# Optimization experiments

Measured on AMD Instinct MI355X. Metric: run time of the kernel, lower is better.

The kernel has to match this reference:

```python
import jax, jax.numpy as jnp
import numpy as np

B, N = 2, 384
NODE_DIM, NODE_HIDDEN, EDGE_DIM = 128, 256, 64
EDGE_H1 = 2 * EDGE_DIM + 2 * NODE_DIM  # 384, forced by concat in edge update
EDGE_H2 = 128
HEADS = 8
SCALE = 1.0 / float(np.sqrt(NODE_HIDDEN // HEADS))  # torch uses node_hidden//heads
EPS = 1e-5


def _w(k, out_dim, in_dim):
    return jax.random.normal(k, (out_dim, in_dim), dtype=jnp.float32) * 0.02


def setup_inputs() -> dict:
    ks = jax.random.split(jax.random.key(0), 32)
    inp = {
        'x': jax.random.normal(ks[0], (B, N, NODE_DIM), dtype=jnp.float32),
        'dense_adj': jax.random.normal(ks[1], (B, N, N, EDGE_DIM), dtype=jnp.float32),
        'wnq': _w(ks[2], NODE_DIM, NODE_DIM),
        'wnk': _w(ks[3], NODE_DIM, NODE_DIM),
        'wnv': _w(ks[4], NODE_DIM, NODE_DIM),
        'weq': _w(ks[5], NODE_DIM, EDGE_DIM),
        'wek': _w(ks[6], NODE_DIM, EDGE_DIM),
        'wev': _w(ks[7], NODE_DIM, EDGE_DIM),
        'nfc1_w': _w(ks[8], NODE_DIM, NODE_DIM),
        'nfc1_b': jnp.zeros((NODE_DIM,), jnp.float32),
        'ln1_g': jnp.ones((NODE_DIM,), jnp.float32),
        'ln1_b': jnp.zeros((NODE_DIM,), jnp.float32),
        'nfc2_w': _w(ks[9], NODE_HIDDEN, NODE_DIM),
        'nfc2_b': jnp.zeros((NODE_HIDDEN,), jnp.float32),
        'nfc3_w': _w(ks[10], NODE_DIM, NODE_HIDDEN),
        'nfc3_b': jnp.zeros((NODE_DIM,), jnp.float32),
        'ln2_g': jnp.ones((NODE_DIM,), jnp.float32),
        'ln2_b': jnp.zeros((NODE_DIM,), jnp.float32),
        'efc1_w': _w(ks[11], EDGE_DIM, EDGE_H1),
        'efc1_b': jnp.zeros((EDGE_DIM,), jnp.float32),
        'efc2_w': _w(ks[12], EDGE_DIM, EDGE_DIM),
        'efc2_b': jnp.zeros((EDGE_DIM,), jnp.float32),
        'eln1_g': jnp.ones((EDGE_DIM,), jnp.float32),
        'eln1_b': jnp.zeros((EDGE_DIM,), jnp.float32),
        'efc3_w': _w(ks[13], EDGE_H2, EDGE_DIM),
        'efc3_b': jnp.zeros((EDGE_H2,), jnp.float32),
        'efc4_w': _w(ks[14], EDGE_DIM, EDGE_H2),
        'efc4_b': jnp.zeros((EDGE_DIM,), jnp.float32),
        'eln2_g': jnp.ones((EDGE_DIM,), jnp.float32),
        'eln2_b': jnp.zeros((EDGE_DIM,), jnp.float32),
    }
    return inp


def layer_norm(t, g, b):
    m = jnp.mean(t, axis=-1, keepdims=True)
    v = jnp.mean((t - m) ** 2, axis=-1, keepdims=True)
    return (t - m) * jax.lax.rsqrt(v + EPS) * g + b


def rt_attention(x, adj, wnq, wnk, wnv, weq, wek, wev):
    Bb, Nn, D = x.shape
    d = D // HEADS
    def sn(t):  # [B,N,D] -> [B,H,N,d]
        return t.reshape(Bb, Nn, HEADS, d).transpose(0, 2, 1, 3)
    def se(t):  # [B,N,N,D] -> [B,H,N,N,d]
        return t.reshape(Bb, Nn, Nn, HEADS, d).transpose(0, 3, 1, 2, 4)
    # edge-augmented per-pair q,k,v: [B,H,i,j,d]
    q = sn(x @ wnq.T)[:, :, :, None, :] + se(adj @ weq.T)
    k = sn(x @ wnk.T)[:, :, None, :, :] + se(adj @ wek.T)
    v = sn(x @ wnv.T)[:, :, None, :, :] + se(adj @ wev.T)
    scores = jnp.sum(q * k, axis=-1) * SCALE          # [B,H,i,j]
    attn = jax.nn.softmax(scores, axis=-1)            # softmax over keys j
    out = jnp.einsum('bhij,bhijc->bhic', attn, v)     # [B,H,N,d]
    # torch reshape_from_batches interleaves as [B,N,d,H] -> [B,N,d*H]
    return out.transpose(0, 2, 3, 1).reshape(Bb, Nn, D)


def reference(x, dense_adj, wnq, wnk, wnv, weq, wek, wev,
              nfc1_w, nfc1_b, ln1_g, ln1_b, nfc2_w, nfc2_b, nfc3_w, nfc3_b,
              ln2_g, ln2_b, efc1_w, efc1_b, efc2_w, efc2_b, eln1_g, eln1_b,
              efc3_w, efc3_b, efc4_w, efc4_b, eln2_g, eln2_b):
    attn_out = rt_attention(x, dense_adj, wnq, wnk, wnv, weq, wek, wev)
    res = attn_out @ nfc1_w.T + nfc1_b
    x = layer_norm(x + res, ln1_g, ln1_b)
    res = jax.nn.relu(x @ nfc2_w.T + nfc2_b) @ nfc3_w.T + nfc3_b
    x = layer_norm(x + res, ln2_g, ln2_b)
    # edge update: [adj_ij, adj_ji, x_j (source), x_i (target)]
    Bb, Nn, D = x.shape
    src = jnp.broadcast_to(x[:, None, :, :], (Bb, Nn, Nn, D))
    tgt = jnp.broadcast_to(x[:, :, None, :], (Bb, Nn, Nn, D))
    rev = jnp.swapaxes(dense_adj, -2, -3)
    ua = jnp.concatenate([dense_adj, rev, src, tgt], axis=-1)  # [B,N,N,EDGE_H1]
    res = jax.nn.relu(ua @ efc1_w.T + efc1_b) @ efc2_w.T + efc2_b
    adj = layer_norm(dense_adj + res, eln1_g, eln1_b)
    res = jax.nn.relu(adj @ efc3_w.T + efc3_b) @ efc4_w.T + efc4_b
    adj = layer_norm(adj + res, eln2_g, eln2_b)
    return (x, adj)
```

## Files before the change

kernel.cpp:

```cpp
#include <hip/hip_runtime.h>
#include <hip/hip_bf16.h>

typedef unsigned short u16;
typedef unsigned int u32;

#define NB 2
#define NN 384
#define ND 128
#define NE 64
#define NHD 8
#define NHID 256
#define EH1 384
#define EH2 128
#define LN_EPS 1e-5f
#define ATT_SCALE 0.17677669529663687f

#define XOUT_ELEMS (NB * NN * ND)
#define ADJ_ELEMS ((size_t)NB * NN * NN * NE)
#define OUT_ELEMS (XOUT_ELEMS + ADJ_ELEMS)
#define SCRATCH_F32 (4 * XOUT_ELEMS)

typedef __attribute__((ext_vector_type(4))) float f32x4;
typedef __attribute__((ext_vector_type(8))) short s16x8;
#define MFMA16(a, b, c) __builtin_amdgcn_mfma_f32_16x16x32_bf16(a, b, c, 0, 0, 0)

__device__ __forceinline__ float bflo(u32 u) {
  return __builtin_bit_cast(float, u << 16);
}
__device__ __forceinline__ float bfhi(u32 u) {
  return __builtin_bit_cast(float, u & 0xffff0000u);
}
__device__ __forceinline__ u16 bfr(float f) {
  return __builtin_bit_cast(u16, __float2bfloat16(f));
}
__device__ __forceinline__ float bfu(u16 h) {
  return __builtin_bit_cast(float, ((u32)h) << 16);
}
__device__ __forceinline__ u32 packbf(float a, float b) {
  return (u32)bfr(a) | ((u32)bfr(b) << 16);
}
__device__ __forceinline__ float wsum64(float v) {
#pragma unroll
  for (int o = 32; o > 0; o >>= 1) v += __shfl_xor(v, o, 64);
  return v;
}
__device__ __forceinline__ float wmax64(float v) {
#pragma unroll
  for (int o = 32; o > 0; o >>= 1) v = fmaxf(v, __shfl_xor(v, o, 64));
  return v;
}

__device__ __forceinline__ s16x8 cvt_frag(const float* p) {
  float4 a = *(const float4*)p;
  float4 c = *(const float4*)(p + 4);
  s16x8 r;
  r[0] = (short)bfr(a.x); r[1] = (short)bfr(a.y);
  r[2] = (short)bfr(a.z); r[3] = (short)bfr(a.w);
  r[4] = (short)bfr(c.x); r[5] = (short)bfr(c.y);
  r[6] = (short)bfr(c.z); r[7] = (short)bfr(c.w);
  return r;
}

__device__ __forceinline__ void cvt8_hl(const float* p, uint4& hi, uint4& lo) {
  float4 a = *(const float4*)p;
  float4 c = *(const float4*)(p + 4);
  float v[8] = {a.x, a.y, a.z, a.w, c.x, c.y, c.z, c.w};
  u32 hw[4], lw[4];
#pragma unroll
  for (int e = 0; e < 4; ++e) {
    u16 h0 = bfr(v[2 * e]), h1 = bfr(v[2 * e + 1]);
    u16 l0 = bfr(v[2 * e] - bfu(h0));
    u16 l1 = bfr(v[2 * e + 1] - bfu(h1));
    hw[e] = (u32)h0 | ((u32)h1 << 16);
    lw[e] = (u32)l0 | ((u32)l1 << 16);
  }
  hi.x = hw[0]; hi.y = hw[1]; hi.z = hw[2]; hi.w = hw[3];
  lo.x = lw[0]; lo.y = lw[1]; lo.z = lw[2]; lo.w = lw[3];
}

__global__ void k_node_qkv(const float* __restrict__ x,
                           const float* __restrict__ wq,
                           const float* __restrict__ wk,
                           const float* __restrict__ wv,
                           float* __restrict__ nq, float* __restrict__ nk,
                           float* __restrict__ nv) {
  int row = blockIdx.x;
  int t = threadIdx.x;
  __shared__ float xs[ND];
  xs[t] = x[row * ND + t];
  __syncthreads();
  float aq = 0.f, ak = 0.f, av = 0.f;
  for (int k = 0; k < ND; ++k) {
    float xv = xs[k];
    aq += xv * wq[t * ND + k];
    ak += xv * wk[t * ND + k];
    av += xv * wv[t * ND + k];
  }
  nq[row * ND + t] = aq;
  nk[row * ND + t] = ak;
  nv[row * ND + t] = av;
}

#define ATJ 128
struct AttnS {
  u16 Ahi[ATJ][NE];
  u16 Alo[ATJ][NE];
  float sc[NHD][NN];
  float psum[NHD][NE];
  float part[4][ND];
};

__global__ void __launch_bounds__(512) k_attn(
    const float* __restrict__ adj,
    const float* __restrict__ weq,
    const float* __restrict__ wek,
    const float* __restrict__ wev,
    const float* __restrict__ nq,
    const float* __restrict__ nk,
    const float* __restrict__ nv,
    float* __restrict__ att) {
  __shared__ AttnS s;
  int bi = blockIdx.x;
  int b = bi / NN;
  int t = threadIdx.x;
  int h = t >> 6;
  int l = t & 63;
  int lr = l & 15, lk = l >> 4;

  s16x8 BQ[2], BK[2];
  {
    const float* wqp = weq + (size_t)(h * 16 + lr) * NE + lk * 8;
    const float* wkp = wek + (size_t)(h * 16 + lr) * NE + lk * 8;
    BQ[0] = cvt_frag(wqp); BQ[1] = cvt_frag(wqp + 32);
    BK[0] = cvt_frag(wkp); BK[1] = cvt_frag(wkp + 32);
  }
  float nqd = nq[(size_t)bi * ND + h * 16 + lr];

  for (int tile = 0; tile < NN / ATJ; ++tile) {
    int jbase = tile * ATJ;
    __syncthreads();
    for (int p = t; p < ATJ * 8; p += 512) {
      int row = p >> 3, u = p & 7;
      const float* src = adj + ((size_t)bi * NN + jbase + row) * NE + u * 8;
      uint4 hi, lo;
      cvt8_hl(src, hi, lo);
      int byt = (row * 128 + u * 16) ^ ((row & 7) << 4);
      *(uint4*)((char*)s.Ahi + byt) = hi;
      *(uint4*)((char*)s.Alo + byt) = lo;
    }
    __syncthreads();

#pragma unroll
    for (int sub = 0; sub < ATJ / 16; ++sub) {
      int trow = sub * 16 + lr;
      int swz = (trow & 7) << 4;
      f32x4 eq = {0.f, 0.f, 0.f, 0.f}, ek = {0.f, 0.f, 0.f, 0.f};
#pragma unroll
      for (int ks = 0; ks < 2; ++ks) {
        int byt = (trow * 128 + ks * 64 + lk * 16) ^ swz;
        s16x8 ah = *(const s16x8*)((const char*)s.Ahi + byt);
        s16x8 al = *(const s16x8*)((const char*)s.Alo + byt);
        eq = MFMA16(ah, BQ[ks], eq);
        eq = MFMA16(al, BQ[ks], eq);
        ek = MFMA16(ah, BK[ks], ek);
        ek = MFMA16(al, BK[ks], ek);
      }
#pragma unroll
      for (int r = 0; r < 4; ++r) {
        int j = jbase + sub * 16 + lk * 4 + r;
        float kv = nk[((size_t)b * NN + j) * ND + h * 16 + lr] + ek[r];
        float prod = (nqd + eq[r]) * kv;
#pragma unroll
        for (int o = 8; o > 0; o >>= 1) prod += __shfl_xor(prod, o, 64);
        if (lr == 0) s.sc[h][j] = prod * ATT_SCALE;
      }
    }
  }
  __syncthreads();

  {
    float vals[NN / 64];
    float m = -1e30f;
#pragma unroll
    for (int r = 0; r < NN / 64; ++r) {
      vals[r] = s.sc[h][l + 64 * r];
      m = fmaxf(m, vals[r]);
    }
    m = wmax64(m);
    float sum = 0.f;
#pragma unroll
    for (int r = 0; r < NN / 64; ++r) {
      vals[r] = __expf(vals[r] - m);
      sum += vals[r];
    }
    sum = wsum64(sum);
    float rinv = 1.f / sum;
#pragma unroll
    for (int r = 0; r < NN / 64; ++r) s.sc[h][l + 64 * r] = vals[r] * rinv;
  }

  {
    float pacc = 0.f;
    const float* ab = adj + (size_t)bi * NN * NE + l;
    const float* prow = s.sc[h];
#pragma unroll 4
    for (int j = 0; j < NN; ++j) pacc += prow[j] * ab[(size_t)j * NE];
    s.psum[h][l] = pacc;
  }
  __syncthreads();

  {
    int c = t & 127, grp = t >> 7;
    int hc = c >> 4;
    float acc = 0.f;
    const float* nvb = nv + (size_t)b * NN * ND + c;
    const float* pr = s.sc[hc];
#pragma unroll 4
    for (int j = grp * (NN / 4); j < (grp + 1) * (NN / 4); ++j)
      acc += pr[j] * nvb[(size_t)j * ND];
    s.part[grp][c] = acc;
  }
  __syncthreads();
  if (t < ND) {
    int c = t, hc = c >> 4;
    float acc = s.part[0][c] + s.part[1][c] + s.part[2][c] + s.part[3][c];
    const float4* wr = (const float4*)(wev + c * NE);
    const float* ps = s.psum[hc];
#pragma unroll
    for (int k4 = 0; k4 < NE / 4; ++k4) {
      float4 w4 = wr[k4];
      acc += w4.x * ps[4 * k4] + w4.y * ps[4 * k4 + 1] +
             w4.z * ps[4 * k4 + 2] + w4.w * ps[4 * k4 + 3];
    }
    att[(size_t)bi * ND + (c & 15) * NHD + hc] = acc;
  }
}

struct FfnS {
  float atts[ND];
  float tvb[ND];
  float x1[ND];
  float hb[NHID];
  float stats[2];
};

__global__ void k_node_ffn(const float* __restrict__ x,
                           const float* __restrict__ att,
                           const float* __restrict__ w1, const float* __restrict__ b1,
                           const float* __restrict__ g1, const float* __restrict__ bb1,
                           const float* __restrict__ w2, const float* __restrict__ b2,
                           const float* __restrict__ w3, const float* __restrict__ b3,
                           const float* __restrict__ g2, const float* __restrict__ bb2,
                           float* __restrict__ xout) {
  __shared__ FfnS s;
  int row = blockIdx.x;
  int tid = threadIdx.x;
  if (tid < ND) s.atts[tid] = att[row * ND + tid];
  __syncthreads();

  if (tid < ND) {
    float acc = b1[tid];
    for (int k = 0; k < ND; ++k) acc += s.atts[k] * w1[tid * ND + k];
    s.tvb[tid] = x[row * ND + tid] + acc;
  }
  __syncthreads();
  if (tid == 0) {
    float m = 0.f;
    for (int k = 0; k < ND; ++k) m += s.tvb[k];
    m *= (1.f / ND);
    float v = 0.f;
    for (int k = 0; k < ND; ++k) { float d = s.tvb[k] - m; v += d * d; }
    s.stats[0] = m;
    s.stats[1] = rsqrtf(v * (1.f / ND) + LN_EPS);
  }
  __syncthreads();
  if (tid < ND)
    s.x1[tid] = (s.tvb[tid] - s.stats[0]) * s.stats[1] * g1[tid] + bb1[tid];
  __syncthreads();

  {
    float acc = b2[tid];
    for (int k = 0; k < ND; ++k) acc += s.x1[k] * w2[tid * ND + k];
    s.hb[tid] = fmaxf(acc, 0.f);
  }
  __syncthreads();

  if (tid < ND) {
    float acc = b3[tid];
    for (int k = 0; k < NHID; ++k) acc += s.hb[k] * w3[tid * NHID + k];
    s.tvb[tid] = s.x1[tid] + acc;
  }
  __syncthreads();
  if (tid == 0) {
    float m = 0.f;
    for (int k = 0; k < ND; ++k) m += s.tvb[k];
    m *= (1.f / ND);
    float v = 0.f;
    for (int k = 0; k < ND; ++k) { float d = s.tvb[k] - m; v += d * d; }
    s.stats[0] = m;
    s.stats[1] = rsqrtf(v * (1.f / ND) + LN_EPS);
  }
  __syncthreads();
  if (tid < ND) {
    float o = (s.tvb[tid] - s.stats[0]) * s.stats[1] * g2[tid] + bb2[tid];
    xout[row * ND + tid] = o;
  }
}

#define EMT 32

struct E1M {
  u16 Ahi[EMT][EH1];
  u16 Alo[EMT][EH1];
  u16 Hhi[EMT][NE];
  u16 Hlo[EMT][NE];
};

__global__ void __launch_bounds__(512) k_edge1(
    const float* __restrict__ adj, const float* __restrict__ xq,
    const float* __restrict__ w1, const float* __restrict__ b1,
    const float* __restrict__ w2, const float* __restrict__ b2,
    const float* __restrict__ g, const float* __restrict__ bb,
    float* __restrict__ adj1out) {
  __shared__ E1M s;
  int bi = blockIdx.x;
  int b = bi / NN, i = bi % NN;
  int t = threadIdx.x;
  int w = t >> 6, l = t & 63;
  int m16 = (w & 1) * 16;
  int n16 = (w >> 1) * 16;
  int lr = l & 15, lk = l >> 4;

  s16x8 B1[12], B2[2];
  {
    const float* wr = w1 + (size_t)(n16 + lr) * EH1 + lk * 8;
#pragma unroll
    for (int ks = 0; ks < 12; ++ks) B1[ks] = cvt_frag(wr + ks * 32);
    const float* w2r = w2 + (size_t)(n16 + lr) * NE + lk * 8;
#pragma unroll
    for (int ks = 0; ks < 2; ++ks) B2[ks] = cvt_frag(w2r + ks * 32);
  }
  float bias1 = b1[n16 + lr];
  float bias2 = b2[n16 + lr];
  float gl = g[l], bl = bb[l];

  for (int mt = 0; mt < NN / EMT; ++mt) {
    int jbase = mt * EMT;
    __syncthreads();
    for (int p = t; p < EMT * 48; p += 512) {
      int row = p / 48, u = p % 48;
      const float* src;
      if (u < 8)
        src = adj + ((size_t)bi * NN + jbase + row) * NE + u * 8;
      else if (u < 16)
        src = adj + ((size_t)(b * NN + jbase + row) * NN + i) * NE + (u - 8) * 8;
      else if (u < 32)
        src = xq + (size_t)(b * NN + jbase + row) * ND + (u - 16) * 8;
      else
        src = xq + (size_t)bi * ND + (u - 32) * 8;
      uint4 hi, lo;
      cvt8_hl(src, hi, lo);
      int byt = (row * 768 + u * 16) ^ ((row & 7) << 4);
      *(uint4*)((char*)s.Ahi + byt) = hi;
      *(uint4*)((char*)s.Alo + byt) = lo;
    }
    __syncthreads();

    f32x4 acc = {0.f, 0.f, 0.f, 0.f};
    int arow = m16 + lr;
    int aswz = (arow & 7) << 4;
#pragma unroll
    for (int ks = 0; ks < 12; ++ks) {
      int byt = (arow * 768 + ks * 64 + lk * 16) ^ aswz;
      s16x8 ah = *(const s16x8*)((const char*)s.Ahi + byt);
      s16x8 al = *(const s16x8*)((const char*)s.Alo + byt);
      acc = MFMA16(ah, B1[ks], acc);
      acc = MFMA16(al, B1[ks], acc);
    }
#pragma unroll
    for (int r = 0; r < 4; ++r) {
      float hv = fmaxf(acc[r] + bias1, 0.f);
      u16 hh = bfr(hv);
      u16 hl = bfr(hv - bfu(hh));
      int row = m16 + lk * 4 + r;
      int byt = (row * 128 + (n16 + lr) * 2) ^ ((row & 7) << 4);
      *(u16*)((char*)s.Hhi + byt) = hh;
      *(u16*)((char*)s.Hlo + byt) = hl;
    }
    __syncthreads();

    f32x4 acc2 = {0.f, 0.f, 0.f, 0.f};
#pragma unroll
    for (int ks = 0; ks < 2; ++ks) {
      int byt = (arow * 128 + ks * 64 + lk * 16) ^ aswz;
      s16x8 ah = *(const s16x8*)((const char*)s.Hhi + byt);
      s16x8 al = *(const s16x8*)((const char*)s.Hlo + byt);
      acc2 = MFMA16(ah, B2[ks], acc2);
      acc2 = MFMA16(al, B2[ks], acc2);
    }
    __syncthreads();
    float* tvb = (float*)s.Hhi;
#pragma unroll
    for (int r = 0; r < 4; ++r) {
      int row = m16 + lk * 4 + r;
      int col = n16 + lr;
      int abyt = (row * 768 + col * 2) ^ ((row & 7) << 4);
      float aorig = bfu(*(const u16*)((const char*)s.Ahi + abyt)) +
                    bfu(*(const u16*)((const char*)s.Alo + abyt));
      tvb[row * NE + col] = aorig + acc2[r] + bias2;
    }
    __syncthreads();
#pragma unroll
    for (int rr = 0; rr < EMT / 8; ++rr) {
      int row = w * (EMT / 8) + rr;
      float tv = tvb[row * NE + l];
      float mean = wsum64(tv) * (1.f / NE);
      float dv = tv - mean;
      float var = wsum64(dv * dv) * (1.f / NE);
      float o = dv * rsqrtf(var + LN_EPS) * gl + bl;
      adj1out[((size_t)bi * NN + jbase + row) * NE + l] = o;
    }
  }
}

struct E2M {
  u16 Ahi[EMT][NE];
  u16 Alo[EMT][NE];
  u16 Hhi[EMT][EH2];
  u16 Hlo[EMT][EH2];
};

__global__ void __launch_bounds__(512) k_edge2(
    float* __restrict__ adjio,
    const float* __restrict__ w3, const float* __restrict__ b3,
    const float* __restrict__ w4, const float* __restrict__ b4,
    const float* __restrict__ g, const float* __restrict__ bb) {
  __shared__ E2M s;
  int bi = blockIdx.x;
  int t = threadIdx.x;
  int w = t >> 6, l = t & 63;
  int m16 = (w & 1) * 16;
  int nb = (w >> 1) * 2;
  int n16 = (w >> 1) * 16;
  int lr = l & 15, lk = l >> 4;

  s16x8 B3[2][2], B4[4];
  {
#pragma unroll
    for (int n = 0; n < 2; ++n) {
      const float* wr = w3 + (size_t)((nb + n) * 16 + lr) * NE + lk * 8;
#pragma unroll
      for (int ks = 0; ks < 2; ++ks) B3[n][ks] = cvt_frag(wr + ks * 32);
    }
    const float* w4r = w4 + (size_t)(n16 + lr) * EH2 + lk * 8;
#pragma unroll
    for (int ks = 0; ks < 4; ++ks) B4[ks] = cvt_frag(w4r + ks * 32);
  }
  float bias3[2] = {b3[nb * 16 + lr], b3[(nb + 1) * 16 + lr]};
  float bias4 = b4[n16 + lr];
  float gl = g[l], bl = bb[l];

  for (int mt = 0; mt < NN / EMT; ++mt) {
    int jbase = mt * EMT;
    __syncthreads();
    for (int p = t; p < EMT * 8; p += 512) {
      int row = p >> 3, u = p & 7;
      const float* src = adjio + ((size_t)bi * NN + jbase + row) * NE + u * 8;
      uint4 hi, lo;
      cvt8_hl(src, hi, lo);
      int byt = (row * 128 + u * 16) ^ ((row & 7) << 4);
      *(uint4*)((char*)s.Ahi + byt) = hi;
      *(uint4*)((char*)s.Alo + byt) = lo;
    }
    __syncthreads();

    f32x4 a3[2] = {{0.f, 0.f, 0.f, 0.f}, {0.f, 0.f, 0.f, 0.f}};
    int arow = m16 + lr;
    int aswz = (arow & 7) << 4;
#pragma unroll
    for (int ks = 0; ks < 2; ++ks) {
      int byt = (arow * 128 + ks * 64 + lk * 16) ^ aswz;
      s16x8 ah = *(const s16x8*)((const char*)s.Ahi + byt);
      s16x8 al = *(const s16x8*)((const char*)s.Alo + byt);
#pragma unroll
      for (int n = 0; n < 2; ++n) {
        a3[n] = MFMA16(ah, B3[n][ks], a3[n]);
        a3[n] = MFMA16(al, B3[n][ks], a3[n]);
      }
    }
#pragma unroll
    for (int n = 0; n < 2; ++n) {
#pragma unroll
      for (int r = 0; r < 4; ++r) {
        float hv = fmaxf(a3[n][r] + bias3[n], 0.f);
        u16 hh = bfr(hv);
        u16 hl = bfr(hv - bfu(hh));
        int row = m16 + lk * 4 + r;
        int byt = (row * 256 + ((nb + n) * 16 + lr) * 2) ^ ((row & 7) << 4);
        *(u16*)((char*)s.Hhi + byt) = hh;
        *(u16*)((char*)s.Hlo + byt) = hl;
      }
    }
    __syncthreads();

    f32x4 a4 = {0.f, 0.f, 0.f, 0.f};
#pragma unroll
    for (int ks = 0; ks < 4; ++ks) {
      int byt = (arow * 256 + ks * 64 + lk * 16) ^ aswz;
      s16x8 ah = *(const s16x8*)((const char*)s.Hhi + byt);
      s16x8 al = *(const s16x8*)((const char*)s.Hlo + byt);
      a4 = MFMA16(ah, B4[ks], a4);
      a4 = MFMA16(al, B4[ks], a4);
    }
    __syncthreads();
    float* tvb = (float*)s.Hhi;
#pragma unroll
    for (int r = 0; r < 4; ++r) {
      int row = m16 + lk * 4 + r;
      int col = n16 + lr;
      int abyt = (row * 128 + col * 2) ^ ((row & 7) << 4);
      float aorig = bfu(*(const u16*)((const char*)s.Ahi + abyt)) +
                    bfu(*(const u16*)((const char*)s.Alo + abyt));
      tvb[row * NE + col] = aorig + a4[r] + bias4;
    }
    __syncthreads();
#pragma unroll
    for (int rr = 0; rr < EMT / 8; ++rr) {
      int row = w * (EMT / 8) + rr;
      float tv = tvb[row * NE + l];
      float mean = wsum64(tv) * (1.f / NE);
      float dv = tv - mean;
      float var = wsum64(dv * dv) * (1.f / NE);
      float o = dv * rsqrtf(var + LN_EPS) * gl + bl;
      adjio[((size_t)bi * NN + jbase + row) * NE + l] = o;
    }
  }
}

extern "C" void kernel_launch(void* const* d_in, const int* in_sizes, int n_in,
                              void* d_out, int out_size, void* d_ws, size_t ws_size,
                              hipStream_t stream) {
  (void)in_sizes; (void)n_in; (void)out_size; (void)d_ws; (void)ws_size;
  const float* x      = (const float*)d_in[0];
  const float* adj    = (const float*)d_in[1];
  const float* wnq    = (const float*)d_in[2];
  const float* wnk    = (const float*)d_in[3];
  const float* wnv    = (const float*)d_in[4];
  const float* weq    = (const float*)d_in[5];
  const float* wek    = (const float*)d_in[6];
  const float* wev    = (const float*)d_in[7];
  const float* nfc1_w = (const float*)d_in[8];
  const float* nfc1_b = (const float*)d_in[9];
  const float* ln1_g  = (const float*)d_in[10];
  const float* ln1_b  = (const float*)d_in[11];
  const float* nfc2_w = (const float*)d_in[12];
  const float* nfc2_b = (const float*)d_in[13];
  const float* nfc3_w = (const float*)d_in[14];
  const float* nfc3_b = (const float*)d_in[15];
  const float* ln2_g  = (const float*)d_in[16];
  const float* ln2_b  = (const float*)d_in[17];
  const float* efc1_w = (const float*)d_in[18];
  const float* efc1_b = (const float*)d_in[19];
  const float* efc2_w = (const float*)d_in[20];
  const float* efc2_b = (const float*)d_in[21];
  const float* eln1_g = (const float*)d_in[22];
  const float* eln1_b = (const float*)d_in[23];
  const float* efc3_w = (const float*)d_in[24];
  const float* efc3_b = (const float*)d_in[25];
  const float* efc4_w = (const float*)d_in[26];
  const float* efc4_b = (const float*)d_in[27];
  const float* eln2_g = (const float*)d_in[28];
  const float* eln2_b = (const float*)d_in[29];

  float* outf = (float*)d_out;
  float* outadj = outf + XOUT_ELEMS;

  float* scratch = outf + OUT_ELEMS - SCRATCH_F32;
  float* nq  = scratch;
  float* nk  = scratch + XOUT_ELEMS;
  float* nv  = scratch + 2 * XOUT_ELEMS;
  float* att = scratch + 3 * XOUT_ELEMS;

  k_node_qkv<<<NB * NN, 128, 0, stream>>>(x, wnq, wnk, wnv, nq, nk, nv);
  k_attn<<<NB * NN, 512, 0, stream>>>(adj, weq, wek, wev, nq, nk, nv, att);
  k_node_ffn<<<NB * NN, 256, 0, stream>>>(x, att, nfc1_w, nfc1_b, ln1_g, ln1_b,
                                          nfc2_w, nfc2_b, nfc3_w, nfc3_b,
                                          ln2_g, ln2_b, outf);
  k_edge1<<<NB * NN, 512, 0, stream>>>(adj, outf, efc1_w, efc1_b, efc2_w, efc2_b,
                                       eln1_g, eln1_b, outadj);
  k_edge2<<<NB * NN, 512, 0, stream>>>(outadj, efc3_w, efc3_b, efc4_w, efc4_b,
                                       eln2_g, eln2_b);
}
```

Baseline: 620.4 us.

## Fuse edge MLP stages into one kernel and fold target-node term into bias

Merges the two edge kernels into a single kernel, so the intermediate layer-normed adjacency stays in shared memory instead of being written to and reread from global memory. It also removes the per-row x_i (target) slice from the efc1 GEMM, since it is constant for a block, and folds it into a per-block bias computed once with a scalar dot product. This cuts efc1 MFMA work by a quarter and removes a full B*N*N*64 fp32 round trip. In exchange the fused kernel holds more weight fragments in registers and uses a larger shared-memory footprint, which may lower occupancy. The folded term uses a bf16-rounded weight with an fp32 x value, so numerics differ slightly from the split hi/lo path.

```diff
diff --git a/kernel.cpp b/kernel.cpp
--- a/kernel.cpp
+++ b/kernel.cpp
@@ -308,84 +308,125 @@
 }
 
 #define EMT 32
-
-struct E1M {
-  u16 Ahi[EMT][EH1];
-  u16 Alo[EMT][EH1];
-  u16 Hhi[EMT][NE];
-  u16 Hlo[EMT][NE];
+struct EFS {
+  u16 Ahi[EMT][128];
+  u16 Alo[EMT][128];
+  union {
+    struct { u16 hi[EMT][128]; u16 lo[EMT][128]; } X;
+    struct { u16 hi[EMT][EH2]; u16 lo[EMT][EH2]; } H2;
+  } u;
+  u16 H1hi[EMT][NE];
+  u16 H1lo[EMT][NE];
+  float Tf[EMT][NE];
+  u16 T1hi[EMT][NE];
+  u16 T1lo[EMT][NE];
 };
 
-__global__ void __launch_bounds__(512) k_edge1(
+__global__ void __launch_bounds__(512) k_edge(
     const float* __restrict__ adj, const float* __restrict__ xq,
     const float* __restrict__ w1, const float* __restrict__ b1,
     const float* __restrict__ w2, const float* __restrict__ b2,
-    const float* __restrict__ g, const float* __restrict__ bb,
-    float* __restrict__ adj1out) {
-  __shared__ E1M s;
+    const float* __restrict__ g1, const float* __restrict__ bb1,
+    const float* __restrict__ w3, const float* __restrict__ b3,
+    const float* __restrict__ w4, const float* __restrict__ b4,
+    const float* __restrict__ g2, const float* __restrict__ bb2,
+    float* __restrict__ adjout) {
+  __shared__ EFS s;
   int bi = blockIdx.x;
   int b = bi / NN, i = bi % NN;
   int t = threadIdx.x;
   int w = t >> 6, l = t & 63;
   int m16 = (w & 1) * 16;
   int n16 = (w >> 1) * 16;
+  int nb = (w >> 1) * 2;
   int lr = l & 15, lk = l >> 4;
 
-  s16x8 B1[12], B2[2];
+  s16x8 B1a[4], B1c[4], B2[2], B3[2][2], B4[4];
   {
     const float* wr = w1 + (size_t)(n16 + lr) * EH1 + lk * 8;
 #pragma unroll
-    for (int ks = 0; ks < 12; ++ks) B1[ks] = cvt_frag(wr + ks * 32);
+    for (int ks = 0; ks < 4; ++ks) {
+      B1a[ks] = cvt_frag(wr + ks * 32);
+      B1c[ks] = cvt_frag(wr + 128 + ks * 32);
+    }
     const float* w2r = w2 + (size_t)(n16 + lr) * NE + lk * 8;
 #pragma unroll
     for (int ks = 0; ks < 2; ++ks) B2[ks] = cvt_frag(w2r + ks * 32);
-  }
-  float bias1 = b1[n16 + lr];
-  float bias2 = b2[n16 + lr];
-  float gl = g[l], bl = bb[l];
+#pragma unroll
+    for (int n = 0; n < 2; ++n) {
+      const float* w3r = w3 + (size_t)((nb + n) * 16 + lr) * NE + lk * 8;
+#pragma unroll
+      for (int ks = 0; ks < 2; ++ks) B3[n][ks] = cvt_frag(w3r + ks * 32);
+    }
+    const float* w4r = w4 + (size_t)(n16 + lr) * EH2 + lk * 8;
+#pragma unroll
+    for (int ks = 0; ks < 4; ++ks) B4[ks] = cvt_frag(w4r + ks * 32);
+  }
+  float b1c;
+  {
+    float ci = 0.f;
+    const float* xr = xq + (size_t)bi * ND;
+    const float* wr = w1 + (size_t)(n16 + lr) * EH1 + 256;
+#pragma unroll 4
+    for (int k = 0; k < ND; ++k) ci += xr[k] * bfu(bfr(wr[k]));
+    b1c = b1[n16 + lr] + ci;
+  }
+  float b2c = b2[n16 + lr];
+  float b3c[2] = {b3[nb * 16 + lr], b3[(nb + 1) * 16 + lr]};
+  float b4c = b4[n16 + lr];
+  float g1l = g1[l], bl1 = bb1[l];
+  float g2l = g2[l], bl2 = bb2[l];
+
+  int arow = m16 + lr;
+  int aswz = (arow & 7) << 4;
 
   for (int mt = 0; mt < NN / EMT; ++mt) {
     int jbase = mt * EMT;
     __syncthreads();
-    for (int p = t; p < EMT * 48; p += 512) {
-      int row = p / 48, u = p % 48;
-      const float* src;
-      if (u < 8)
-        src = adj + ((size_t)bi * NN + jbase + row) * NE + u * 8;
-      else if (u < 16)
-        src = adj + ((size_t)(b * NN + jbase + row) * NN + i) * NE + (u - 8) * 8;
-      else if (u < 32)
-        src = xq + (size_t)(b * NN + jbase + row) * ND + (u - 16) * 8;
-      else
-        src = xq + (size_t)bi * ND + (u - 32) * 8;
-      uint4 hi, lo;
-      cvt8_hl(src, hi, lo);
-      int byt = (row * 768 + u * 16) ^ ((row & 7) << 4);
-      *(uint4*)((char*)s.Ahi + byt) = hi;
-      *(uint4*)((char*)s.Alo + byt) = lo;
+    for (int p = t; p < EMT * 32; p += 512) {
+      int row = p >> 5, uu = p & 31;
+      if (uu < 16) {
+        const float* src = (uu < 8)
+            ? adj + ((size_t)bi * NN + jbase + row) * NE + uu * 8
+            : adj + ((size_t)(b * NN + jbase + row) * NN + i) * NE + (uu - 8) * 8;
+        uint4 hi, lo;
+        cvt8_hl(src, hi, lo);
+        int byt = (row * 256 + uu * 16) ^ ((row & 7) << 4);
+        *(uint4*)((char*)s.Ahi + byt) = hi;
+        *(uint4*)((char*)s.Alo + byt) = lo;
+      } else {
+        const float* src = xq + (size_t)(b * NN + jbase + row) * ND + (uu - 16) * 8;
+        uint4 hi, lo;
+        cvt8_hl(src, hi, lo);
+        int byt = (row * 256 + (uu - 16) * 16) ^ ((row & 7) << 4);
+        *(uint4*)((char*)s.u.X.hi + byt) = hi;
+        *(uint4*)((char*)s.u.X.lo + byt) = lo;
+      }
     }
     __syncthreads();
 
     f32x4 acc = {0.f, 0.f, 0.f, 0.f};
-    int arow = m16 + lr;
-    int aswz = (arow & 7) << 4;
-#pragma unroll
-    for (int ks = 0; ks < 12; ++ks) {
-      int byt = (arow * 768 + ks * 64 + lk * 16) ^ aswz;
+#pragma unroll
+    for (int ks = 0; ks < 4; ++ks) {
+      int byt = (arow * 256 + ks * 64 + lk * 16) ^ aswz;
       s16x8 ah = *(const s16x8*)((const char*)s.Ahi + byt);
       s16x8 al = *(const s16x8*)((const char*)s.Alo + byt);
-      acc = MFMA16(ah, B1[ks], acc);
-      acc = MFMA16(al, B1[ks], acc);
+      acc = MFMA16(ah, B1a[ks], acc);
+      acc = MFMA16(al, B1a[ks], acc);
+      s16x8 xh = *(const s16x8*)((const char*)s.u.X.hi + byt);
+      s16x8 xl = *(const s16x8*)((const char*)s.u.X.lo + byt);
+      acc = MFMA16(xh, B1c[ks], acc);
+      acc = MFMA16(xl, B1c[ks], acc);
     }
 #pragma unroll
     for (int r = 0; r < 4; ++r) {
-      float hv = fmaxf(acc[r] + bias1, 0.f);
+      int row = m16 + lk * 4 + r;
+      float hv = fmaxf(acc[r] + b1c, 0.f);
       u16 hh = bfr(hv);
       u16 hl = bfr(hv - bfu(hh));
-      int row = m16 + lk * 4 + r;
       int byt = (row * 128 + (n16 + lr) * 2) ^ ((row & 7) << 4);
-      *(u16*)((char*)s.Hhi + byt) = hh;
-      *(u16*)((char*)s.Hlo + byt) = hl;
+      *(u16*)((char*)s.H1hi + byt) = hh;
+      *(u16*)((char*)s.H1lo + byt) = hl;
     }
     __syncthreads();
 
@@ -393,95 +434,45 @@
 #pragma unroll
     for (int ks = 0; ks < 2; ++ks) {
       int byt = (arow * 128 + ks * 64 + lk * 16) ^ aswz;
-      s16x8 ah = *(const s16x8*)((const char*)s.Hhi + byt);
-      s16x8 al = *(const s16x8*)((const char*)s.Hlo + byt);
+      s16x8 ah = *(const s16x8*)((const char*)s.H1hi + byt);
+      s16x8 al = *(const s16x8*)((const char*)s.H1lo + byt);
       acc2 = MFMA16(ah, B2[ks], acc2);
       acc2 = MFMA16(al, B2[ks], acc2);
     }
-    __syncthreads();
-    float* tvb = (float*)s.Hhi;
 #pragma unroll
     for (int r = 0; r < 4; ++r) {
       int row = m16 + lk * 4 + r;
       int col = n16 + lr;
-      int abyt = (row * 768 + col * 2) ^ ((row & 7) << 4);
+      int abyt = (row * 256 + col * 2) ^ ((row & 7) << 4);
       float aorig = bfu(*(const u16*)((const char*)s.Ahi + abyt)) +
                     bfu(*(const u16*)((const char*)s.Alo + abyt));
-      tvb[row * NE + col] = aorig + acc2[r] + bias2;
-    }
-    __syncthreads();
+      s.Tf[row][col] = aorig + acc2[r] + b2c;
+    }
+    __syncthreads();
+
 #pragma unroll
     for (int rr = 0; rr < EMT / 8; ++rr) {
       int row = w * (EMT / 8) + rr;
-      float tv = tvb[row * NE + l];
+      float tv = s.Tf[row][l];
       float mean = wsum64(tv) * (1.f / NE);
       float dv = tv - mean;
       float var = wsum64(dv * dv) * (1.f / NE);
-      float o = dv * rsqrtf(var + LN_EPS) * gl + bl;
-      adj1out[((size_t)bi * NN + jbase + row) * NE + l] = o;
-    }
-  }
-}
-
-struct E2M {
-  u16 Ahi[EMT][NE];
-  u16 Alo[EMT][NE];
-  u16 Hhi[EMT][EH2];
-  u16 Hlo[EMT][EH2];
-};
-
-__global__ void __launch_bounds__(512) k_edge2(
-    float* __restrict__ adjio,
-    const float* __restrict__ w3, const float* __restrict__ b3,
-    const float* __restrict__ w4, const float* __restrict__ b4,
-    const float* __restrict__ g, const float* __restrict__ bb) {
-  __shared__ E2M s;
-  int bi = blockIdx.x;
-  int t = threadIdx.x;
-  int w = t >> 6, l = t & 63;
-  int m16 = (w & 1) * 16;
-  int nb = (w >> 1) * 2;
-  int n16 = (w >> 1) * 16;
-  int lr = l & 15, lk = l >> 4;
-
-  s16x8 B3[2][2], B4[4];
-  {
-#pragma unroll
-    for (int n = 0; n < 2; ++n) {
-      const float* wr = w3 + (size_t)((nb + n) * 16 + lr) * NE + lk * 8;
-#pragma unroll
-      for (int ks = 0; ks < 2; ++ks) B3[n][ks] = cvt_frag(wr + ks * 32);
-    }
-    const float* w4r = w4 + (size_t)(n16 + lr) * EH2 + lk * 8;
-#pragma unroll
-    for (int ks = 0; ks < 4; ++ks) B4[ks] = cvt_frag(w4r + ks * 32);
-  }
-  float bias3[2] = {b3[nb * 16 + lr], b3[(nb + 1) * 16 + lr]};
-  float bias4 = b4[n16 + lr];
-  float gl = g[l], bl = bb[l];
-
-  for (int mt = 0; mt < NN / EMT; ++mt) {
-    int jbase = mt * EMT;
-    __syncthreads();
-    for (int p = t; p < EMT * 8; p += 512) {
-      int row = p >> 3, u = p & 7;
-      const float* src = adjio + ((size_t)bi * NN + jbase + row) * NE + u * 8;
-      uint4 hi, lo;
-      cvt8_hl(src, hi, lo);
-      int byt = (row * 128 + u * 16) ^ ((row & 7) << 4);
-      *(uint4*)((char*)s.Ahi + byt) = hi;
-      *(uint4*)((char*)s.Alo + byt) = lo;
+      float o = dv * rsqrtf(var + LN_EPS) * g1l + bl1;
+      s.Tf[row][l] = o;
+      u16 oh = bfr(o);
+      u16 ol = bfr(o - bfu(oh));
+      int byt = (row * 128 + l * 2) ^ ((row & 7) << 4);
+      *(u16*)((char*)s.T1hi + byt) = oh;
+      *(u16*)((char*)s.T1lo + byt) = ol;
     }
     __syncthreads();
 
     f32x4 a3[2] = {{0.f, 0.f, 0.f, 0.f}, {0.f, 0.f, 0.f, 0.f}};
-    int arow = m16 + lr;
-    int aswz = (arow & 7) << 4;
 #pragma unroll
     for (int ks = 0; ks < 2; ++ks) {
       int byt = (arow * 128 + ks * 64 + lk * 16) ^ aswz;
-      s16x8 ah = *(const s16x8*)((const char*)s.Ahi + byt);
-      s16x8 al = *(const s16x8*)((const char*)s.Alo + byt);
+      s16x8 ah = *(const s16x8*)((const char*)s.T1hi + byt);
+      s16x8 al = *(const s16x8*)((const char*)s.T1lo + byt);
 #pragma unroll
       for (int n = 0; n < 2; ++n) {
         a3[n] = MFMA16(ah, B3[n][ks], a3[n]);
@@ -492,13 +483,13 @@
     for (int n = 0; n < 2; ++n) {
 #pragma unroll
       for (int r = 0; r < 4; ++r) {
-        float hv = fmaxf(a3[n][r] + bias3[n], 0.f);
+        float hv = fmaxf(a3[n][r] + b3c[n], 0.f);
         u16 hh = bfr(hv);
         u16 hl = bfr(hv - bfu(hh));
         int row = m16 + lk * 4 + r;
         int byt = (row * 256 + ((nb + n) * 16 + lr) * 2) ^ ((row & 7) << 4);
-        *(u16*)((char*)s.Hhi + byt) = hh;
-        *(u16*)((char*)s.Hlo + byt) = hl;
+        *(u16*)((char*)s.u.H2.hi + byt) = hh;
+        *(u16*)((char*)s.u.H2.lo + byt) = hl;
       }
     }
     __syncthreads();
@@ -507,32 +498,28 @@
 #pragma unroll
     for (int ks = 0; ks < 4; ++ks) {
       int byt = (arow * 256 + ks * 64 + lk * 16) ^ aswz;
-      s16x8 ah = *(const s16x8*)((const char*)s.Hhi + byt);
-      s16x8 al = *(const s16x8*)((const char*)s.Hlo + byt);
+      s16x8 ah = *(const s16x8*)((const char*)s.u.H2.hi + byt);
+      s16x8 al = *(const s16x8*)((const char*)s.u.H2.lo + byt);
       a4 = MFMA16(ah, B4[ks], a4);
       a4 = MFMA16(al, B4[ks], a4);
     }
-    __syncthreads();
-    float* tvb = (float*)s.Hhi;
 #pragma unroll
     for (int r = 0; r < 4; ++r) {
       int row = m16 + lk * 4 + r;
       int col = n16 + lr;
-      int abyt = (row * 128 + col * 2) ^ ((row & 7) << 4);
-      float aorig = bfu(*(const u16*)((const char*)s.Ahi + abyt)) +
-                    bfu(*(const u16*)((const char*)s.Alo + abyt));
-      tvb[row * NE + col] = aorig + a4[r] + bias4;
-    }
-    __syncthreads();
+      s.Tf[row][col] = s.Tf[row][col] + a4[r] + b4c;
+    }
+    __syncthreads();
+
 #pragma unroll
     for (int rr = 0; rr < EMT / 8; ++rr) {
       int row = w * (EMT / 8) + rr;
-      float tv = tvb[row * NE + l];
+      float tv = s.Tf[row][l];
       float mean = wsum64(tv) * (1.f / NE);
       float dv = tv - mean;
       float var = wsum64(dv * dv) * (1.f / NE);
-      float o = dv * rsqrtf(var + LN_EPS) * gl + bl;
-      adjio[((size_t)bi * NN + jbase + row) * NE + l] = o;
+      float o = dv * rsqrtf(var + LN_EPS) * g2l + bl2;
+      adjout[((size_t)bi * NN + jbase + row) * NE + l] = o;
     }
   }
 }
@@ -586,8 +573,8 @@
   k_node_ffn<<<NB * NN, 256, 0, stream>>>(x, att, nfc1_w, nfc1_b, ln1_g, ln1_b,
                                           nfc2_w, nfc2_b, nfc3_w, nfc3_b,
                                           ln2_g, ln2_b, outf);
-  k_edge1<<<NB * NN, 512, 0, stream>>>(adj, outf, efc1_w, efc1_b, efc2_w, efc2_b,
-                                       eln1_g, eln1_b, outadj);
-  k_edge2<<<NB * NN, 512, 0, stream>>>(outadj, efc3_w, efc3_b, efc4_w, efc4_b,
-                                       eln2_g, eln2_b);
-}
+  k_edge<<<NB * NN, 512, 0, stream>>>(adj, outf, efc1_w, efc1_b,
+                                      efc2_w, efc2_b, eln1_g, eln1_b,
+                                      efc3_w, efc3_b, efc4_w, efc4_b,
+                                      eln2_g, eln2_b, outadj);
+}
```

After: 723.9 us. +16.7%, slower.
